# Performance work log

Measured on AMD Instinct MI355X. Metric: run time of the kernel, lower is better.

The kernel has to match this reference:

```python
import jax, jax.numpy as jnp
import numpy as np

E = 8        # number of part experts
D_IN = 3     # coordinate dim
H = 256      # hidden width (3 hidden layers)
D_OUT = 1


def setup_inputs() -> dict:
    key = jax.random.key(0)
    ks = jax.random.split(key, 9)
    # coords in [-1, 1]
    coords = jax.random.uniform(ks[0], (100000, D_IN), jnp.float32, -1.0, 1.0)
    def glorot(k, shape):
        fan_in, fan_out = shape[-2], shape[-1]
        s = jnp.sqrt(2.0 / (fan_in + fan_out)).astype(jnp.float32)
        return jax.random.normal(k, shape, jnp.float32) * s
    W0 = glorot(ks[1], (E, D_IN, H)); b0 = jnp.zeros((E, H), jnp.float32)
    W1 = glorot(ks[2], (E, H, H));    b1 = jnp.zeros((E, H), jnp.float32)
    W2 = glorot(ks[3], (E, H, H));    b2 = jnp.zeros((E, H), jnp.float32)
    W3 = glorot(ks[4], (E, H, D_OUT)); b3 = jnp.zeros((E, D_OUT), jnp.float32)
    return {"coords": coords, "W0": W0, "b0": b0, "W1": W1, "b1": b1,
            "W2": W2, "b2": b2, "W3": W3, "b3": b3}


def reference(coords, W0, b0, W1, b1, W2, b2, W3, b3):
    # All E experts consume the SAME coords; batch them as grouped GEMMs.
    # h: [E, N, H]
    h = jax.nn.relu(jnp.einsum('nd,edh->enh', coords, W0) + b0[:, None, :])
    h = jax.nn.relu(jnp.einsum('enh,ehk->enk', h, W1) + b1[:, None, :])
    h = jax.nn.relu(jnp.einsum('enh,ehk->enk', h, W2) + b2[:, None, :])
    expert_out = jnp.einsum('enh,eho->eno', h, W3) + b3[:, None, :]  # [E, N, 1]
    # torch.stack(expert_tensors).max(dim=0).values
    max_occ = jnp.max(expert_out, axis=0)  # [N, 1]
    return max_occ
```

## Files before the change

### kernel.cpp

```cpp
#include <hip/hip_runtime.h>
#include <hip/hip_bf16.h>

#define NE 8
#define HD 256
#define NT 64
#define NTHREADS 512
#define WPITCH 32
#define SLICE_ELEMS (HD * WPITCH)

typedef __attribute__((ext_vector_type(8))) short short8;
typedef __attribute__((ext_vector_type(4))) float f32x4;

__device__ __forceinline__ unsigned short f2bf_u16(float f) {
    union { __hip_bfloat16 b; unsigned short u; } v;
    v.b = __float2bfloat16(f);
    return v.u;
}
__device__ __forceinline__ unsigned int pack2bf(float lo, float hi) {
    return (unsigned int)f2bf_u16(lo) | ((unsigned int)f2bf_u16(hi) << 16);
}
__device__ __forceinline__ void bfsplit(float v, unsigned short& hi, unsigned short& lo) {
    hi = f2bf_u16(v);
    union { unsigned int u; float f; } c; c.u = ((unsigned int)hi) << 16;
    lo = f2bf_u16(v - c.f);
}
__device__ __forceinline__ int swz(int row, int col) {
    return row * HD + (col ^ ((row & 7) << 3));
}

__global__ void prep_weights(const float* __restrict__ W1, const float* __restrict__ W2,
                             unsigned short* __restrict__ W1p, unsigned short* __restrict__ W2p) {
    int idx = blockIdx.x * blockDim.x + threadIdx.x;
    const int TOT = NE * 8 * SLICE_ELEMS;
    if (idx >= TOT) return;
    int kk = idx & 31;
    int n  = (idx >> 5) & 255;
    int s  = (idx >> 13) & 7;
    int e  = idx >> 16;
    int k = s * 32 + kk;
    W1p[idx] = f2bf_u16(W1[(e * HD + k) * HD + n]);
    W2p[idx] = f2bf_u16(W2[(e * HD + k) * HD + n]);
}

__global__ void prep_w0(const float* __restrict__ W0, const float* __restrict__ b0,
                        unsigned short* __restrict__ W0k) {
    int idx = blockIdx.x * blockDim.x + threadIdx.x;
    if (idx >= NE * HD) return;
    int n = idx & 255, e = idx >> 8;
    float wx = W0[(e*3+0)*HD + n], wy = W0[(e*3+1)*HD + n], wz = W0[(e*3+2)*HD + n];
    float bb = b0[e*HD + n];
    unsigned short xh,xl,yh,yl,zh,zl,bh,bl;
    bfsplit(wx,xh,xl); bfsplit(wy,yh,yl); bfsplit(wz,zh,zl); bfsplit(bb,bh,bl);
    unsigned short s[32] = {xh,xh,xl, yh,yh,yl, zh,zh,zl, bh,bl};
    unsigned short* dst = W0k + idx * 32;
    #pragma unroll
    for (int i = 0; i < 32; ++i) dst[i] = s[i];
}

__device__ __forceinline__ void stage_slice(const unsigned short* __restrict__ gsrc,
                                            unsigned short* lbase, int g, int lane) {
    const char* gp = (const char*)gsrc + g * 4096 + lane * 16;
    char* l = (char*)lbase + g * 4096;
    #pragma unroll
    for (int i = 0; i < 4; ++i)
        __builtin_amdgcn_global_load_lds(
            (const __attribute__((address_space(1))) unsigned int*)(gp + i * 1024),
            (__attribute__((address_space(3))) unsigned int*)(l + i * 1024),
            16, 0, 0);
}

#define KSLICE_BODY(CURBUF)                                                                  \
    {                                                                                        \
        const unsigned short* Ar = (CURBUF) + (g*64 + l15) * WPITCH + kg*8;                  \
        short8 af0 = *(const short8*)(Ar + 0*16*WPITCH);                                     \
        short8 af1 = *(const short8*)(Ar + 1*16*WPITCH);                                     \
        short8 af2 = *(const short8*)(Ar + 2*16*WPITCH);                                     \
        short8 af3 = *(const short8*)(Ar + 3*16*WPITCH);                                     \
        const int k0 = s*32 + kg*8;                                                          \
        _Pragma("unroll")                                                                    \
        for (int nt = 0; nt < 2; ++nt) {                                                     \
            short8 bf = *(const short8*)(Act + swz(h*32 + nt*16 + l15, k0));                 \
            acc[0][nt] = __builtin_amdgcn_mfma_f32_16x16x32_bf16(af0, bf, acc[0][nt], 0,0,0);\
            acc[1][nt] = __builtin_amdgcn_mfma_f32_16x16x32_bf16(af1, bf, acc[1][nt], 0,0,0);\
            acc[2][nt] = __builtin_amdgcn_mfma_f32_16x16x32_bf16(af2, bf, acc[2][nt], 0,0,0);\
            acc[3][nt] = __builtin_amdgcn_mfma_f32_16x16x32_bf16(af3, bf, acc[3][nt], 0,0,0);\
        }                                                                                    \
    }

__global__ __launch_bounds__(NTHREADS, 2) void moe_expert(
    const float* __restrict__ coords, int npts,
    const unsigned short* __restrict__ W0k, const float* __restrict__ b1,
    const unsigned short* __restrict__ W1p,
    const unsigned short* __restrict__ W2p, const float* __restrict__ b2,
    const float* __restrict__ W3, const float* __restrict__ b3,
    float* __restrict__ ws)
{
    __shared__ __align__(16) unsigned short Act[NT * HD];
    __shared__ __align__(16) unsigned short WbA[SLICE_ELEMS];
    __shared__ __align__(16) unsigned short WbB[SLICE_ELEMS];
    __shared__ __align__(16) unsigned short cbufK[NT * 32];
    __shared__ float pscr[NT * 4];

    const int t = threadIdx.x;
    const int lane = t & 63;
    const int w = t >> 6;
    const int g = w >> 1;
    const int h = w & 1;
    const int l15 = lane & 15;
    const int kg = lane >> 4;
    const int e = blockIdx.x & 7;
    const int p0 = (blockIdx.x >> 3) * NT;

    const unsigned short* W0e = W0k + e * SLICE_ELEMS;
    const unsigned short* W1e = W1p + e * 8 * SLICE_ELEMS;
    const unsigned short* W2e = W2p + e * 8 * SLICE_ELEMS;

    if (h == 0) stage_slice(W0e, WbB, g, lane);
    if (t < NT) {
        int p = p0 + t;
        int pc = p < npts ? p : npts - 1;
        float x = coords[pc*3], y = coords[pc*3+1], z = coords[pc*3+2];
        unsigned short xh,xl,yh,yl,zh,zl;
        bfsplit(x,xh,xl); bfsplit(y,yh,yl); bfsplit(z,zh,zl);
        const unsigned short ONE = 0x3F80;
        union { unsigned short s[32]; uint4 q[4]; } pk;
        #pragma unroll
        for (int i = 0; i < 32; ++i) pk.s[i] = 0;
        pk.s[0]=xh; pk.s[1]=xl; pk.s[2]=xh;
        pk.s[3]=yh; pk.s[4]=yl; pk.s[5]=yh;
        pk.s[6]=zh; pk.s[7]=zl; pk.s[8]=zh;
        pk.s[9]=ONE; pk.s[10]=ONE;
        uint4* dst = (uint4*)(cbufK + t * 32);
        dst[0]=pk.q[0]; dst[1]=pk.q[1]; dst[2]=pk.q[2]; dst[3]=pk.q[3];
    }
    f32x4 b1v[4];
    #pragma unroll
    for (int mt = 0; mt < 4; ++mt)
        b1v[mt] = *(const f32x4*)(b1 + e*HD + g*64 + mt*16 + kg*4);
    __syncthreads();

    f32x4 acc[4][2];
    #pragma unroll
    for (int mt = 0; mt < 4; ++mt)
        #pragma unroll
        for (int nt = 0; nt < 2; ++nt)
            acc[mt][nt] = (f32x4){0.f, 0.f, 0.f, 0.f};

    if (h == 0) stage_slice(W1e, WbA, g, lane);
    {
        const unsigned short* Ar = WbB + (g*64 + l15) * WPITCH + kg*8;
        short8 af0 = *(const short8*)(Ar + 0*16*WPITCH);
        short8 af1 = *(const short8*)(Ar + 1*16*WPITCH);
        short8 af2 = *(const short8*)(Ar + 2*16*WPITCH);
        short8 af3 = *(const short8*)(Ar + 3*16*WPITCH);
        #pragma unroll
        for (int nt = 0; nt < 2; ++nt) {
            short8 bf = *(const short8*)(cbufK + (h*32 + nt*16 + l15) * 32 + kg*8);
            acc[0][nt] = __builtin_amdgcn_mfma_f32_16x16x32_bf16(af0, bf, acc[0][nt], 0,0,0);
            acc[1][nt] = __builtin_amdgcn_mfma_f32_16x16x32_bf16(af1, bf, acc[1][nt], 0,0,0);
            acc[2][nt] = __builtin_amdgcn_mfma_f32_16x16x32_bf16(af2, bf, acc[2][nt], 0,0,0);
            acc[3][nt] = __builtin_amdgcn_mfma_f32_16x16x32_bf16(af3, bf, acc[3][nt], 0,0,0);
        }
        #pragma unroll
        for (int mt = 0; mt < 4; ++mt)
            #pragma unroll
            for (int nt = 0; nt < 2; ++nt) {
                const int p = h*32 + nt*16 + l15;
                const int n0 = g*64 + mt*16 + kg*4;
                unsigned int lo = pack2bf(fmaxf(acc[mt][nt][0], 0.f),
                                          fmaxf(acc[mt][nt][1], 0.f));
                unsigned int hi = pack2bf(fmaxf(acc[mt][nt][2], 0.f),
                                          fmaxf(acc[mt][nt][3], 0.f));
                *(uint2*)(Act + swz(p, n0)) = make_uint2(lo, hi);
            }
    }
    __syncthreads();

    #pragma unroll
    for (int mt = 0; mt < 4; ++mt)
        #pragma unroll
        for (int nt = 0; nt < 2; ++nt)
            acc[mt][nt] = (f32x4){0.f, 0.f, 0.f, 0.f};

    #pragma unroll
    for (int s = 0; s < 8; ++s) {
        unsigned short* cur = (s & 1) ? WbB : WbA;
        unsigned short* nxt = (s & 1) ? WbA : WbB;
        if (h == 0) {
            if (s < 7) stage_slice(W1e + (s+1) * SLICE_ELEMS, nxt, g, lane);
            else       stage_slice(W2e, nxt, g, lane);
        }
        KSLICE_BODY(cur)
        __syncthreads();
    }

    #pragma unroll
    for (int mt = 0; mt < 4; ++mt) {
        const int n0 = g*64 + mt*16 + kg*4;
        const f32x4 bb = b1v[mt];
        #pragma unroll
        for (int nt = 0; nt < 2; ++nt) {
            const int p = h*32 + nt*16 + l15;
            unsigned int lo = pack2bf(fmaxf(acc[mt][nt][0] + bb[0], 0.f),
                                      fmaxf(acc[mt][nt][1] + bb[1], 0.f));
            unsigned int hi = pack2bf(fmaxf(acc[mt][nt][2] + bb[2], 0.f),
                                      fmaxf(acc[mt][nt][3] + bb[3], 0.f));
            *(uint2*)(Act + swz(p, n0)) = make_uint2(lo, hi);
        }
    }
    __syncthreads();

    #pragma unroll
    for (int mt = 0; mt < 4; ++mt)
        #pragma unroll
        for (int nt = 0; nt < 2; ++nt)
            acc[mt][nt] = (f32x4){0.f, 0.f, 0.f, 0.f};

    #pragma unroll
    for (int s = 0; s < 8; ++s) {
        unsigned short* cur = (s & 1) ? WbB : WbA;
        unsigned short* nxt = (s & 1) ? WbA : WbB;
        if (h == 0 && s < 7) stage_slice(W2e + (s+1) * SLICE_ELEMS, nxt, g, lane);
        KSLICE_BODY(cur)
        if (s < 7) __syncthreads();
    }

    {
        f32x4 bbv[4], w3v[4];
        #pragma unroll
        for (int mt = 0; mt < 4; ++mt) {
            const int nb = g*64 + mt*16 + kg*4;
            bbv[mt] = *(const f32x4*)(b2 + e*HD + nb);
            w3v[mt] = *(const f32x4*)(W3 + e*HD + nb);
        }
        #pragma unroll
        for (int nt = 0; nt < 2; ++nt) {
            float s = 0.f;
            #pragma unroll
            for (int mt = 0; mt < 4; ++mt)
                #pragma unroll
                for (int r = 0; r < 4; ++r)
                    s += fmaxf(acc[mt][nt][r] + bbv[mt][r], 0.f) * w3v[mt][r];
            s += __shfl_xor(s, 16);
            s += __shfl_xor(s, 32);
            if (kg == 0) pscr[(h*32 + nt*16 + l15) * 4 + g] = s;
        }
    }
    __syncthreads();
    if (t < NT) {
        f32x4 v = *(const f32x4*)(pscr + t * 4);
        int p = p0 + t;
        if (p < npts) ws[e * npts + p] = v[0] + v[1] + v[2] + v[3] + b3[e];
    }
}

__global__ void moe_reduce(const float* __restrict__ ws, float* __restrict__ out, int npts) {
    int p = blockIdx.x * 256 + threadIdx.x;
    if (p >= npts) return;
    float m = ws[p];
    #pragma unroll
    for (int e = 1; e < NE; ++e) m = fmaxf(m, ws[e * npts + p]);
    out[p] = m;
}

extern "C" void kernel_launch(void* const* d_in, const int* in_sizes, int n_in,
                              void* d_out, int out_size, void* d_ws, size_t ws_size,
                              hipStream_t stream) {
    const float* coords = (const float*)d_in[0];
    const float* W0 = (const float*)d_in[1];
    const float* b0 = (const float*)d_in[2];
    const float* W1 = (const float*)d_in[3];
    const float* b1 = (const float*)d_in[4];
    const float* W2 = (const float*)d_in[5];
    const float* b2 = (const float*)d_in[6];
    const float* W3 = (const float*)d_in[7];
    const float* b3 = (const float*)d_in[8];
    const int npts = in_sizes[0] / 3;

    unsigned short* W1p = (unsigned short*)d_ws;
    unsigned short* W2p = W1p + NE * 8 * SLICE_ELEMS;
    unsigned short* W0k = W2p + NE * 8 * SLICE_ELEMS;
    float* eout = (float*)(W0k + NE * SLICE_ELEMS);

    const int PREP_TOT = NE * 8 * SLICE_ELEMS;
    prep_weights<<<(PREP_TOT + 255) / 256, 256, 0, stream>>>(W1, W2, W1p, W2p);
    prep_w0<<<(NE * HD + 255) / 256, 256, 0, stream>>>(W0, b0, W0k);

    int ntiles = (npts + NT - 1) / NT;
    moe_expert<<<ntiles * NE, NTHREADS, 0, stream>>>(
        coords, npts, W0k, b1, W1p, W2p, b2, W3, b3, eout);

    moe_reduce<<<(npts + 255) / 256, 256, 0, stream>>>(eout, (float*)d_out, npts);
}
```

Before: 272.7 us.

## Halve block to 256 threads, single weight buffer, wider per-wave tiles for occupancy

Block size drops from 512 to 256 threads. Each wave now computes all 64 points (4 n-tiles) instead of 32. The double-buffered weight slices become one buffer, and cbufK and pscr are merged into a shared aux region. Together these cut LDS use so three blocks can fit per CU. The cost is that weight staging is no longer overlapped with MFMA work: each slice is now loaded and then waited on with extra barriers. The larger accumulator array also raises register pressure.

```diff
diff --git a/kernel.cpp b/kernel.cpp
--- a/kernel.cpp
+++ b/kernel.cpp
@@ -4,7 +4,7 @@
 #define NE 8
 #define HD 256
 #define NT 64
-#define NTHREADS 512
+#define NTHREADS 256
 #define WPITCH 32
 #define SLICE_ELEMS (HD * WPITCH)
 
@@ -69,17 +69,17 @@
             16, 0, 0);
 }
 
-#define KSLICE_BODY(CURBUF)                                                                  \
+#define KSLICE_BODY(CURBUF, K0)                                                              \
     {                                                                                        \
         const unsigned short* Ar = (CURBUF) + (g*64 + l15) * WPITCH + kg*8;                  \
         short8 af0 = *(const short8*)(Ar + 0*16*WPITCH);                                     \
         short8 af1 = *(const short8*)(Ar + 1*16*WPITCH);                                     \
         short8 af2 = *(const short8*)(Ar + 2*16*WPITCH);                                     \
         short8 af3 = *(const short8*)(Ar + 3*16*WPITCH);                                     \
-        const int k0 = s*32 + kg*8;                                                          \
+        const int k0 = (K0) + kg*8;                                                          \
         _Pragma("unroll")                                                                    \
-        for (int nt = 0; nt < 2; ++nt) {                                                     \
-            short8 bf = *(const short8*)(Act + swz(h*32 + nt*16 + l15, k0));                 \
+        for (int nt = 0; nt < 4; ++nt) {                                                     \
+            short8 bf = *(const short8*)(Act + swz(nt*16 + l15, k0));                        \
             acc[0][nt] = __builtin_amdgcn_mfma_f32_16x16x32_bf16(af0, bf, acc[0][nt], 0,0,0);\
             acc[1][nt] = __builtin_amdgcn_mfma_f32_16x16x32_bf16(af1, bf, acc[1][nt], 0,0,0);\
             acc[2][nt] = __builtin_amdgcn_mfma_f32_16x16x32_bf16(af2, bf, acc[2][nt], 0,0,0);\
@@ -87,7 +87,14 @@
         }                                                                                    \
     }
 
-__global__ __launch_bounds__(NTHREADS, 2) void moe_expert(
+#define ACC_CLEAR()                                           \
+    _Pragma("unroll")                                         \
+    for (int mt = 0; mt < 4; ++mt)                            \
+        _Pragma("unroll")                                     \
+        for (int nt = 0; nt < 4; ++nt)                        \
+            acc[mt][nt] = (f32x4){0.f, 0.f, 0.f, 0.f};
+
+__global__ __launch_bounds__(NTHREADS, 3) void moe_expert(
     const float* __restrict__ coords, int npts,
     const unsigned short* __restrict__ W0k, const float* __restrict__ b1,
     const unsigned short* __restrict__ W1p,
@@ -96,16 +103,14 @@
     float* __restrict__ ws)
 {
     __shared__ __align__(16) unsigned short Act[NT * HD];
-    __shared__ __align__(16) unsigned short WbA[SLICE_ELEMS];
-    __shared__ __align__(16) unsigned short WbB[SLICE_ELEMS];
-    __shared__ __align__(16) unsigned short cbufK[NT * 32];
-    __shared__ float pscr[NT * 4];
+    __shared__ __align__(16) unsigned short Wb[SLICE_ELEMS];
+    __shared__ __align__(16) unsigned char aux[NT * 32 * 2];
+    unsigned short* cbufK = (unsigned short*)aux;
+    float* pscr = (float*)aux;
 
     const int t = threadIdx.x;
     const int lane = t & 63;
-    const int w = t >> 6;
-    const int g = w >> 1;
-    const int h = w & 1;
+    const int g = t >> 6;
     const int l15 = lane & 15;
     const int kg = lane >> 4;
     const int e = blockIdx.x & 7;
@@ -115,7 +120,7 @@
     const unsigned short* W1e = W1p + e * 8 * SLICE_ELEMS;
     const unsigned short* W2e = W2p + e * 8 * SLICE_ELEMS;
 
-    if (h == 0) stage_slice(W0e, WbB, g, lane);
+    stage_slice(W0e, Wb, g, lane);
     if (t < NT) {
         int p = p0 + t;
         int pc = p < npts ? p : npts - 1;
@@ -139,23 +144,18 @@
         b1v[mt] = *(const f32x4*)(b1 + e*HD + g*64 + mt*16 + kg*4);
     __syncthreads();
 
-    f32x4 acc[4][2];
-    #pragma unroll
-    for (int mt = 0; mt < 4; ++mt)
-        #pragma unroll
-        for (int nt = 0; nt < 2; ++nt)
-            acc[mt][nt] = (f32x4){0.f, 0.f, 0.f, 0.f};
-
-    if (h == 0) stage_slice(W1e, WbA, g, lane);
+    f32x4 acc[4][4];
+    ACC_CLEAR()
+
     {
-        const unsigned short* Ar = WbB + (g*64 + l15) * WPITCH + kg*8;
+        const unsigned short* Ar = Wb + (g*64 + l15) * WPITCH + kg*8;
         short8 af0 = *(const short8*)(Ar + 0*16*WPITCH);
         short8 af1 = *(const short8*)(Ar + 1*16*WPITCH);
         short8 af2 = *(const short8*)(Ar + 2*16*WPITCH);
         short8 af3 = *(const short8*)(Ar + 3*16*WPITCH);
         #pragma unroll
-        for (int nt = 0; nt < 2; ++nt) {
-            short8 bf = *(const short8*)(cbufK + (h*32 + nt*16 + l15) * 32 + kg*8);
+        for (int nt = 0; nt < 4; ++nt) {
+            short8 bf = *(const short8*)(cbufK + (nt*16 + l15) * 32 + kg*8);
             acc[0][nt] = __builtin_amdgcn_mfma_f32_16x16x32_bf16(af0, bf, acc[0][nt], 0,0,0);
             acc[1][nt] = __builtin_amdgcn_mfma_f32_16x16x32_bf16(af1, bf, acc[1][nt], 0,0,0);
             acc[2][nt] = __builtin_amdgcn_mfma_f32_16x16x32_bf16(af2, bf, acc[2][nt], 0,0,0);
@@ -164,8 +164,8 @@
         #pragma unroll
         for (int mt = 0; mt < 4; ++mt)
             #pragma unroll
-            for (int nt = 0; nt < 2; ++nt) {
-                const int p = h*32 + nt*16 + l15;
+            for (int nt = 0; nt < 4; ++nt) {
+                const int p = nt*16 + l15;
                 const int n0 = g*64 + mt*16 + kg*4;
                 unsigned int lo = pack2bf(fmaxf(acc[mt][nt][0], 0.f),
                                           fmaxf(acc[mt][nt][1], 0.f));
@@ -175,32 +175,27 @@
             }
     }
     __syncthreads();
-
-    #pragma unroll
-    for (int mt = 0; mt < 4; ++mt)
-        #pragma unroll
-        for (int nt = 0; nt < 2; ++nt)
-            acc[mt][nt] = (f32x4){0.f, 0.f, 0.f, 0.f};
-
+    stage_slice(W1e, Wb, g, lane);
+    __syncthreads();
+
+    ACC_CLEAR()
     #pragma unroll
     for (int s = 0; s < 8; ++s) {
-        unsigned short* cur = (s & 1) ? WbB : WbA;
-        unsigned short* nxt = (s & 1) ? WbA : WbB;
-        if (h == 0) {
-            if (s < 7) stage_slice(W1e + (s+1) * SLICE_ELEMS, nxt, g, lane);
-            else       stage_slice(W2e, nxt, g, lane);
-        }
-        KSLICE_BODY(cur)
+        KSLICE_BODY(Wb, s*32)
         __syncthreads();
-    }
-
+        if (s < 7) {
+            stage_slice(W1e + (s+1) * SLICE_ELEMS, Wb, g, lane);
+            __syncthreads();
+        }
+    }
+    stage_slice(W2e, Wb, g, lane);
     #pragma unroll
     for (int mt = 0; mt < 4; ++mt) {
         const int n0 = g*64 + mt*16 + kg*4;
         const f32x4 bb = b1v[mt];
         #pragma unroll
-        for (int nt = 0; nt < 2; ++nt) {
-            const int p = h*32 + nt*16 + l15;
+        for (int nt = 0; nt < 4; ++nt) {
+            const int p = nt*16 + l15;
             unsigned int lo = pack2bf(fmaxf(acc[mt][nt][0] + bb[0], 0.f),
                                       fmaxf(acc[mt][nt][1] + bb[1], 0.f));
             unsigned int hi = pack2bf(fmaxf(acc[mt][nt][2] + bb[2], 0.f),
@@ -210,19 +205,15 @@
     }
     __syncthreads();
 
-    #pragma unroll
-    for (int mt = 0; mt < 4; ++mt)
-        #pragma unroll
-        for (int nt = 0; nt < 2; ++nt)
-            acc[mt][nt] = (f32x4){0.f, 0.f, 0.f, 0.f};
-
+    ACC_CLEAR()
     #pragma unroll
     for (int s = 0; s < 8; ++s) {
-        unsigned short* cur = (s & 1) ? WbB : WbA;
-        unsigned short* nxt = (s & 1) ? WbA : WbB;
-        if (h == 0 && s < 7) stage_slice(W2e + (s+1) * SLICE_ELEMS, nxt, g, lane);
-        KSLICE_BODY(cur)
-        if (s < 7) __syncthreads();
+        KSLICE_BODY(Wb, s*32)
+        if (s < 7) {
+            __syncthreads();
+            stage_slice(W2e + (s+1) * SLICE_ELEMS, Wb, g, lane);
+            __syncthreads();
+        }
     }
 
     {
@@ -233,8 +224,9 @@
             bbv[mt] = *(const f32x4*)(b2 + e*HD + nb);
             w3v[mt] = *(const f32x4*)(W3 + e*HD + nb);
         }
-        #pragma unroll
-        for (int nt = 0; nt < 2; ++nt) {
+        __syncthreads();
+        #pragma unroll
+        for (int nt = 0; nt < 4; ++nt) {
             float s = 0.f;
             #pragma unroll
             for (int mt = 0; mt < 4; ++mt)
@@ -243,7 +235,7 @@
                     s += fmaxf(acc[mt][nt][r] + bbv[mt][r], 0.f) * w3v[mt][r];
             s += __shfl_xor(s, 16);
             s += __shfl_xor(s, 32);
-            if (kg == 0) pscr[(h*32 + nt*16 + l15) * 4 + g] = s;
+            if (kg == 0) pscr[(nt*16 + l15) * 4 + g] = s;
         }
     }
     __syncthreads();
```

Result: faster. 244.2 us (-10.4%).
